# Kernel optimization log

Hardware: AMD Instinct MI355X
Metric: run time of the kernel (lower is better)

## Reference

```python
import jax, jax.numpy as jnp
import numpy as np

N_NODES = 50000
N_EDGES = 600000
D = 128


def _gcn_layer(h, W, b, src, dst, norm, n_nodes):
    # symmetric-normalized GCN conv: D^{-1/2} A D^{-1/2} H W + b
    h = h * norm[:, None]                                  # [N, d] scale by src norm
    msgs = h[src]                                          # [E, d] gather
    agg = jax.ops.segment_sum(msgs, dst, num_segments=n_nodes)  # [N, d] scatter-add
    agg = agg * norm[:, None]                              # scale by dst norm
    return agg @ W + b


def setup_inputs() -> dict:
    key = jax.random.key(0)
    kf, ks, kd, kw0, kw1 = jax.random.split(key, 5)
    features = jax.random.normal(kf, (N_NODES, D), dtype=jnp.float32)
    src = jax.random.randint(ks, (N_EDGES,), 0, N_NODES)
    dst = jax.random.randint(kd, (N_EDGES,), 0, N_NODES)
    scale = 1.0 / np.sqrt(D)
    W0 = jax.random.normal(kw0, (D, D), dtype=jnp.float32) * scale
    W1 = jax.random.normal(kw1, (D, D), dtype=jnp.float32) * scale
    b0 = jnp.zeros((D,), dtype=jnp.float32)
    b1 = jnp.zeros((D,), dtype=jnp.float32)
    return {"features": features, "src": src, "dst": dst,
            "W0": W0, "b0": b0, "W1": W1, "b1": b1}


def reference(features, src, dst, W0, b0, W1, b1):
    n_nodes = features.shape[0]
    # symmetric norm from in-degree (self-degree clamp to avoid div by zero)
    deg = jax.ops.segment_sum(jnp.ones_like(dst, dtype=features.dtype), dst,
                              num_segments=n_nodes)
    norm = jax.lax.rsqrt(jnp.maximum(deg, 1.0))
    h = _gcn_layer(features, W0, b0, src, dst, norm, n_nodes)
    h = jax.nn.relu(h)
    h = _gcn_layer(h, W1, b1, src, dst, norm, n_nodes)
    return h
```

## Files before the change

kernel.cpp:

```cpp
#include <hip/hip_runtime.h>
#include <hip/hip_bf16.h>

#define D 128
#define CAP 48

typedef short bf16x8 __attribute__((ext_vector_type(8)));
typedef float f32x4 __attribute__((ext_vector_type(4)));

__device__ inline ushort f2bf(float v) {
    __hip_bfloat16 h = __float2bfloat16(v);
    return *reinterpret_cast<ushort*>(&h);
}
__device__ inline float bflo(uint v) { return __uint_as_float(v << 16); }
__device__ inline float bfhi(uint v) { return __uint_as_float(v & 0xffff0000u); }
__device__ inline uint pk2(float lo, float hi) {
    return (uint)f2bf(lo) | ((uint)f2bf(hi) << 16);
}


__global__ void init_cursor_kernel(int* __restrict__ cursor, int n) {
    int g = blockIdx.x * 256 + threadIdx.x;
    if (g < n) cursor[g] = g * CAP;
}

__global__ void scatter_edges_kernel(const int* __restrict__ src, const int* __restrict__ dst,
                                     int* __restrict__ cursor, int* __restrict__ bucket, int E) {
    int e = blockIdx.x * 256 + threadIdx.x;
    if (e < E) {
        int d = dst[e];
        int slot = atomicAdd(&cursor[d], 1);
        bucket[slot] = src[e];
    }
}

__global__ __launch_bounds__(256) void prep_kernel(
    const float4* __restrict__ x, const int* __restrict__ cursor,
    float* __restrict__ normv, uint2* __restrict__ xs,
    const float* __restrict__ W0, const float* __restrict__ W1,
    ushort* __restrict__ Wt0, ushort* __restrict__ Wt1, int n_nodes) {
    int tid = threadIdx.x;
    if (blockIdx.x < 32) {
#pragma unroll
        for (int kk = 0; kk < 4; ++kk) {
            int idx = blockIdx.x * 1024 + kk * 256 + tid;
            const float* W = (idx < 16384) ? W0 : W1;
            ushort* Wt = (idx < 16384) ? Wt0 : Wt1;
            int e = idx & 16383;
            int n = e >> 7, k = e & 127;
            Wt[e] = f2bf(W[k * 128 + n]);
        }
        return;
    }
    int total = n_nodes * 32;
    int stride = (gridDim.x - 32) * 256;
    for (int i = (blockIdx.x - 32) * 256 + tid; i < total; i += stride) {
        int row = i >> 5;
        float dg = (float)(cursor[row] - row * CAP);
        float nn = rsqrtf(fmaxf(dg, 1.0f));
        if ((i & 31) == 0) normv[row] = nn;
        float4 v = x[i];
        uint2 o;
        o.x = pk2(v.x * nn, v.y * nn);
        o.y = pk2(v.z * nn, v.w * nn);
        xs[i] = o;
    }
}

__global__ __launch_bounds__(256) void gather_bf16_kernel(
    const ushort* __restrict__ x, const float* __restrict__ normv,
    const int* __restrict__ cursor, const int* __restrict__ bucket,
    ushort* __restrict__ out, int n_nodes) {
    int node = (blockIdx.x * 256 + threadIdx.x) >> 6;
    if (node >= n_nodes) return;
    int lane = threadIdx.x & 63;
    int grp = lane >> 4;
    int l16 = lane & 15;
    int e0 = node * CAP;
    int e1 = cursor[node];
    const uint4* xp = (const uint4*)x;

    float a[8] = {0.f, 0.f, 0.f, 0.f, 0.f, 0.f, 0.f, 0.f};
    int e = e0 + grp;
    for (; e + 8 < e1; e += 12) {
        int s0 = bucket[e];
        int s1 = bucket[e + 4];
        int s2 = bucket[e + 8];
        uint4 v0 = xp[(size_t)s0 * 16 + l16];
        uint4 v1 = xp[(size_t)s1 * 16 + l16];
        uint4 v2 = xp[(size_t)s2 * 16 + l16];
        a[0] += bflo(v0.x); a[1] += bfhi(v0.x);
        a[2] += bflo(v0.y); a[3] += bfhi(v0.y);
        a[4] += bflo(v0.z); a[5] += bfhi(v0.z);
        a[6] += bflo(v0.w); a[7] += bfhi(v0.w);
        a[0] += bflo(v1.x); a[1] += bfhi(v1.x);
        a[2] += bflo(v1.y); a[3] += bfhi(v1.y);
        a[4] += bflo(v1.z); a[5] += bfhi(v1.z);
        a[6] += bflo(v1.w); a[7] += bfhi(v1.w);
        a[0] += bflo(v2.x); a[1] += bfhi(v2.x);
        a[2] += bflo(v2.y); a[3] += bfhi(v2.y);
        a[4] += bflo(v2.z); a[5] += bfhi(v2.z);
        a[6] += bflo(v2.w); a[7] += bfhi(v2.w);
    }
    for (; e < e1; e += 4) {
        int s = bucket[e];
        uint4 v = xp[(size_t)s * 16 + l16];
        a[0] += bflo(v.x); a[1] += bfhi(v.x);
        a[2] += bflo(v.y); a[3] += bfhi(v.y);
        a[4] += bflo(v.z); a[5] += bfhi(v.z);
        a[6] += bflo(v.w); a[7] += bfhi(v.w);
    }

#pragma unroll
    for (int j = 0; j < 8; ++j) {
        a[j] += __shfl_xor(a[j], 16, 64);
        a[j] += __shfl_xor(a[j], 32, 64);
    }

    if (grp == 0) {
        float nn = normv[node];
        uint4 o;
        o.x = pk2(a[0] * nn, a[1] * nn);
        o.y = pk2(a[2] * nn, a[3] * nn);
        o.z = pk2(a[4] * nn, a[5] * nn);
        o.w = pk2(a[6] * nn, a[7] * nn);
        ((uint4*)out)[(size_t)node * 16 + l16] = o;
    }
}

template <bool LAYER1>
__global__ __launch_bounds__(256) void mfma_matmul_kernel(
    const ushort* __restrict__ A, const ushort* __restrict__ Wt,
    const float* __restrict__ bias, const float* __restrict__ normv,
    void* outp, int n_nodes) {
    __shared__ ushort Ws[128 * 136];
    int tid = threadIdx.x;

#pragma unroll
    for (int i = 0; i < 8; ++i) {
        int e = (i * 256 + tid) * 8;
        int r = e >> 7, c = e & 127;
        *(uint4*)&Ws[r * 136 + c] = *(const uint4*)&Wt[e];
    }
    __syncthreads();

    int w = tid >> 6, lane = tid & 63;
    int n16 = lane & 15, g = lane >> 4;
    int rowbase = blockIdx.x * 64 + w * 16;
    int arow = rowbase + n16;

    const bf16x8 zero8 = {0, 0, 0, 0, 0, 0, 0, 0};
    bf16x8 a[4];
    bool aok = (arow < n_nodes);
#pragma unroll
    for (int kk = 0; kk < 4; ++kk)
        a[kk] = aok ? *(const bf16x8*)&A[(size_t)arow * 128 + kk * 32 + g * 8] : zero8;

    float bvals[8];
#pragma unroll
    for (int j = 0; j < 8; ++j) bvals[j] = bias[j * 16 + n16];

    f32x4 acc[8];
#pragma unroll
    for (int j = 0; j < 8; ++j) acc[j] = (f32x4){0.f, 0.f, 0.f, 0.f};

#pragma unroll
    for (int kk = 0; kk < 4; ++kk) {
#pragma unroll
        for (int j = 0; j < 8; ++j) {
            bf16x8 b = *(const bf16x8*)&Ws[(j * 16 + n16) * 136 + kk * 32 + g * 8];
            acc[j] = __builtin_amdgcn_mfma_f32_16x16x32_bf16(a[kk], b, acc[j], 0, 0, 0);
        }
    }

    int rloc = g * 4;
#pragma unroll
    for (int r = 0; r < 4; ++r) {
        int row = rowbase + rloc + r;
        if (row >= n_nodes) continue;
        if (LAYER1) {
            float nn = normv[row];
            ushort* ob = (ushort*)outp;
#pragma unroll
            for (int j = 0; j < 8; ++j) {
                float v = fmaxf(acc[j][r] + bvals[j], 0.f) * nn;
                ob[(size_t)row * 128 + j * 16 + n16] = f2bf(v);
            }
        } else {
            float* of = (float*)outp;
#pragma unroll
            for (int j = 0; j < 8; ++j)
                of[(size_t)row * 128 + j * 16 + n16] = acc[j][r] + bvals[j];
        }
    }
}


extern "C" void kernel_launch(void* const* d_in, const int* in_sizes, int n_in,
                              void* d_out, int out_size, void* d_ws, size_t ws_size,
                              hipStream_t stream) {
    const float* features = (const float*)d_in[0];
    const int*   src      = (const int*)d_in[1];
    const int*   dst      = (const int*)d_in[2];
    const float* W0       = (const float*)d_in[3];
    const float* b0       = (const float*)d_in[4];
    const float* W1       = (const float*)d_in[5];
    const float* b1       = (const float*)d_in[6];
    float* out = (float*)d_out;

    const int N = in_sizes[0] / D;
    const int E = in_sizes[1];

    char* ws = (char*)d_ws;
    size_t off = 0;
    auto take = [&](size_t bytes) {
        char* p = ws + off;
        off = (off + bytes + 255) & ~(size_t)255;
        return p;
    };
    int*    cursor = (int*)take((size_t)N * 4);
    float*  normv  = (float*)take((size_t)N * 4);
    int*    bucket = (int*)take((size_t)N * CAP * 4);
    ushort* Wt0    = (ushort*)take(16384 * 2);
    ushort* Wt1    = (ushort*)take(16384 * 2);
    ushort* xs     = (ushort*)take((size_t)N * D * 2);
    ushort* buf1   = (ushort*)d_out;

    int NB = (N + 255) / 256;
    int EB = (E + 255) / 256;
    int GB = (N + 3) / 4;
    int MB = (N + 63) / 64;

    init_cursor_kernel<<<NB, 256, 0, stream>>>(cursor, N);
    scatter_edges_kernel<<<EB, 256, 0, stream>>>(src, dst, cursor, bucket, E);
    prep_kernel<<<32 + 2048, 256, 0, stream>>>((const float4*)features, cursor, normv,
                                               (uint2*)xs, W0, W1, Wt0, Wt1, N);

    gather_bf16_kernel<<<GB, 256, 0, stream>>>(xs, normv, cursor, bucket, buf1, N);
    mfma_matmul_kernel<true><<<MB, 256, 0, stream>>>(buf1, Wt0, b0, normv, buf1, N);
    gather_bf16_kernel<<<GB, 256, 0, stream>>>(buf1, normv, cursor, bucket, xs, N);
    mfma_matmul_kernel<false><<<MB, 256, 0, stream>>>(xs, Wt1, b1, nullptr, out, N);
}
```

Measured before the change: 123.8 us.

## Pad per-node atomic counters to 64 bytes and store bucket sources as uint16

Each per-node cursor now sits in its own 64-byte slot (stride 16 ints) and holds a relative count instead of an absolute offset. The intent is to cut atomic contention and false sharing during edge bucketing. Bucket entries shrink from int32 to uint16 source indices, halving the bucket footprint and the index-load traffic in both gathers. Storing sources as uint16 cannot represent node ids of 65536 or more, so it only works because N is 50000. The padded cursor array also makes the count reads in prep and gather strided and uncoalesced.

```diff
diff --git a/kernel.cpp b/kernel.cpp
--- a/kernel.cpp
+++ b/kernel.cpp
@@ -18,23 +18,24 @@
 }
 
 
-__global__ void init_cursor_kernel(int* __restrict__ cursor, int n) {
+__global__ void init_cursor_kernel(int* __restrict__ cursor16, int n) {
     int g = blockIdx.x * 256 + threadIdx.x;
-    if (g < n) cursor[g] = g * CAP;
+    if (g < n) cursor16[g * 16] = 0;
 }
 
 __global__ void scatter_edges_kernel(const int* __restrict__ src, const int* __restrict__ dst,
-                                     int* __restrict__ cursor, int* __restrict__ bucket, int E) {
+                                     int* __restrict__ cursor16, ushort* __restrict__ bucket,
+                                     int E) {
     int e = blockIdx.x * 256 + threadIdx.x;
     if (e < E) {
         int d = dst[e];
-        int slot = atomicAdd(&cursor[d], 1);
-        bucket[slot] = src[e];
+        int c = atomicAdd(&cursor16[d * 16], 1);
+        bucket[d * CAP + c] = (ushort)src[e];
     }
 }
 
 __global__ __launch_bounds__(256) void prep_kernel(
-    const float4* __restrict__ x, const int* __restrict__ cursor,
+    const float4* __restrict__ x, const int* __restrict__ cursor16,
     float* __restrict__ normv, uint2* __restrict__ xs,
     const float* __restrict__ W0, const float* __restrict__ W1,
     ushort* __restrict__ Wt0, ushort* __restrict__ Wt1, int n_nodes) {
@@ -55,7 +56,7 @@
     int stride = (gridDim.x - 32) * 256;
     for (int i = (blockIdx.x - 32) * 256 + tid; i < total; i += stride) {
         int row = i >> 5;
-        float dg = (float)(cursor[row] - row * CAP);
+        float dg = (float)cursor16[row * 16];
         float nn = rsqrtf(fmaxf(dg, 1.0f));
         if ((i & 31) == 0) normv[row] = nn;
         float4 v = x[i];
@@ -68,7 +69,7 @@
 
 __global__ __launch_bounds__(256) void gather_bf16_kernel(
     const ushort* __restrict__ x, const float* __restrict__ normv,
-    const int* __restrict__ cursor, const int* __restrict__ bucket,
+    const int* __restrict__ cursor16, const ushort* __restrict__ bucket,
     ushort* __restrict__ out, int n_nodes) {
     int node = (blockIdx.x * 256 + threadIdx.x) >> 6;
     if (node >= n_nodes) return;
@@ -76,7 +77,7 @@
     int grp = lane >> 4;
     int l16 = lane & 15;
     int e0 = node * CAP;
-    int e1 = cursor[node];
+    int e1 = e0 + cursor16[node * 16];
     const uint4* xp = (const uint4*)x;
 
     float a[8] = {0.f, 0.f, 0.f, 0.f, 0.f, 0.f, 0.f, 0.f};
@@ -217,26 +218,26 @@
         off = (off + bytes + 255) & ~(size_t)255;
         return p;
     };
-    int*    cursor = (int*)take((size_t)N * 4);
-    float*  normv  = (float*)take((size_t)N * 4);
-    int*    bucket = (int*)take((size_t)N * CAP * 4);
-    ushort* Wt0    = (ushort*)take(16384 * 2);
-    ushort* Wt1    = (ushort*)take(16384 * 2);
-    ushort* xs     = (ushort*)take((size_t)N * D * 2);
-    ushort* buf1   = (ushort*)d_out;
+    int*    cursor16 = (int*)take((size_t)N * 64);
+    float*  normv    = (float*)take((size_t)N * 4);
+    ushort* bucket   = (ushort*)take((size_t)N * CAP * 2);
+    ushort* Wt0      = (ushort*)take(16384 * 2);
+    ushort* Wt1      = (ushort*)take(16384 * 2);
+    ushort* xs       = (ushort*)take((size_t)N * D * 2);
+    ushort* buf1     = (ushort*)d_out;
 
     int NB = (N + 255) / 256;
     int EB = (E + 255) / 256;
     int GB = (N + 3) / 4;
     int MB = (N + 63) / 64;
 
-    init_cursor_kernel<<<NB, 256, 0, stream>>>(cursor, N);
-    scatter_edges_kernel<<<EB, 256, 0, stream>>>(src, dst, cursor, bucket, E);
-    prep_kernel<<<32 + 2048, 256, 0, stream>>>((const float4*)features, cursor, normv,
+    init_cursor_kernel<<<NB, 256, 0, stream>>>(cursor16, N);
+    scatter_edges_kernel<<<EB, 256, 0, stream>>>(src, dst, cursor16, bucket, E);
+    prep_kernel<<<32 + 2048, 256, 0, stream>>>((const float4*)features, cursor16, normv,
                                                (uint2*)xs, W0, W1, Wt0, Wt1, N);
 
-    gather_bf16_kernel<<<GB, 256, 0, stream>>>(xs, normv, cursor, bucket, buf1, N);
+    gather_bf16_kernel<<<GB, 256, 0, stream>>>(xs, normv, cursor16, bucket, buf1, N);
     mfma_matmul_kernel<true><<<MB, 256, 0, stream>>>(buf1, Wt0, b0, normv, buf1, N);
-    gather_bf16_kernel<<<GB, 256, 0, stream>>>(buf1, normv, cursor, bucket, xs, N);
+    gather_bf16_kernel<<<GB, 256, 0, stream>>>(buf1, normv, cursor16, bucket, xs, N);
     mfma_matmul_kernel<false><<<MB, 256, 0, stream>>>(xs, Wt1, b1, nullptr, out, N);
 }
```

Result: slower. 126.5 us (+2.2%).

## Replace global-atomic edge bucketing with two-level LDS binning and 16-bit indices

Applied to the files above, without the earlier changes.

Edge bucketing by destination used to be one global atomic per edge. It now runs in two passes. The first pass bins edges per block into segments keyed by 256-node ranges, counted with shared-memory atomics. The second pass places each range's edges into per-node buckets with LDS atomics and writes per-node degree. Bucket source indices and the packed segment entries are stored as 16-bit values, which halves index traffic in the gathers but only works while the node count fits in 16 bits. Edges past the fixed segment or bucket capacities are silently dropped, and degree is clamped to the bucket capacity.

```diff
diff --git a/kernel.cpp b/kernel.cpp
--- a/kernel.cpp
+++ b/kernel.cpp
@@ -3,6 +3,9 @@
 
 #define D 128
 #define CAP 48
+#define SB 128
+#define SEGCAP 64
+#define RB 256
 
 typedef short bf16x8 __attribute__((ext_vector_type(8)));
 typedef float f32x4 __attribute__((ext_vector_type(4)));
@@ -17,24 +20,57 @@
     return (uint)f2bf(lo) | ((uint)f2bf(hi) << 16);
 }
 
-
-__global__ void init_cursor_kernel(int* __restrict__ cursor, int n) {
-    int g = blockIdx.x * 256 + threadIdx.x;
-    if (g < n) cursor[g] = g * CAP;
-}
-
-__global__ void scatter_edges_kernel(const int* __restrict__ src, const int* __restrict__ dst,
-                                     int* __restrict__ cursor, int* __restrict__ bucket, int E) {
-    int e = blockIdx.x * 256 + threadIdx.x;
-    if (e < E) {
+__global__ __launch_bounds__(256) void bin_edges_kernel(
+    const int* __restrict__ src, const int* __restrict__ dst,
+    uint* __restrict__ seg, int* __restrict__ cnt, int E, int nr) {
+    __shared__ int lcnt[256];
+    __shared__ int lcur[256];
+    int tid = threadIdx.x, b = blockIdx.x;
+    lcnt[tid] = 0;
+    __syncthreads();
+    int ce = (E + SB - 1) / SB;
+    int ebeg = b * ce, eend = min(ebeg + ce, E);
+    for (int e = ebeg + tid; e < eend; e += 256)
+        atomicAdd(&lcnt[dst[e] >> 8], 1);
+    __syncthreads();
+    lcur[tid] = 0;
+    if (tid < nr) cnt[b * 256 + tid] = lcnt[tid];
+    __syncthreads();
+    for (int e = ebeg + tid; e < eend; e += 256) {
         int d = dst[e];
-        int slot = atomicAdd(&cursor[d], 1);
-        bucket[slot] = src[e];
-    }
+        int r = d >> 8;
+        int c = atomicAdd(&lcur[r], 1);
+        if (c < SEGCAP)
+            seg[(r * SB + b) * SEGCAP + c] = (uint)src[e] | ((uint)(d & 255) << 16);
+    }
+}
+
+__global__ __launch_bounds__(256) void scatter_local_kernel(
+    const uint* __restrict__ seg, const int* __restrict__ cnt,
+    ushort* __restrict__ bucket, int* __restrict__ degv, int n_nodes) {
+    __shared__ int lc[256];
+    int tid = threadIdx.x, r = blockIdx.x;
+    lc[tid] = 0;
+    __syncthreads();
+    int sub = tid >> 5, lane = tid & 31;
+    for (int b = sub; b < SB; b += 8) {
+        int n = min(cnt[b * 256 + r], SEGCAP);
+        int base = (r * SB + b) * SEGCAP;
+        for (int i = lane; i < n; i += 32) {
+            uint u = seg[base + i];
+            int ldst = u >> 16;
+            int s = u & 0xffff;
+            int c = atomicAdd(&lc[ldst], 1);
+            if (c < CAP) bucket[(r * RB + ldst) * CAP + c] = (ushort)s;
+        }
+    }
+    __syncthreads();
+    int node = r * RB + tid;
+    if (node < n_nodes) degv[node] = min(lc[tid], CAP);
 }
 
 __global__ __launch_bounds__(256) void prep_kernel(
-    const float4* __restrict__ x, const int* __restrict__ cursor,
+    const float4* __restrict__ x, const int* __restrict__ degv,
     float* __restrict__ normv, uint2* __restrict__ xs,
     const float* __restrict__ W0, const float* __restrict__ W1,
     ushort* __restrict__ Wt0, ushort* __restrict__ Wt1, int n_nodes) {
@@ -55,7 +91,7 @@
     int stride = (gridDim.x - 32) * 256;
     for (int i = (blockIdx.x - 32) * 256 + tid; i < total; i += stride) {
         int row = i >> 5;
-        float dg = (float)(cursor[row] - row * CAP);
+        float dg = (float)degv[row];
         float nn = rsqrtf(fmaxf(dg, 1.0f));
         if ((i & 31) == 0) normv[row] = nn;
         float4 v = x[i];
@@ -68,7 +104,7 @@
 
 __global__ __launch_bounds__(256) void gather_bf16_kernel(
     const ushort* __restrict__ x, const float* __restrict__ normv,
-    const int* __restrict__ cursor, const int* __restrict__ bucket,
+    const int* __restrict__ degv, const ushort* __restrict__ bucket,
     ushort* __restrict__ out, int n_nodes) {
     int node = (blockIdx.x * 256 + threadIdx.x) >> 6;
     if (node >= n_nodes) return;
@@ -76,7 +112,7 @@
     int grp = lane >> 4;
     int l16 = lane & 15;
     int e0 = node * CAP;
-    int e1 = cursor[node];
+    int e1 = e0 + degv[node];
     const uint4* xp = (const uint4*)x;
 
     float a[8] = {0.f, 0.f, 0.f, 0.f, 0.f, 0.f, 0.f, 0.f};
@@ -209,6 +245,7 @@
 
     const int N = in_sizes[0] / D;
     const int E = in_sizes[1];
+    const int NR = (N + RB - 1) / RB;
 
     char* ws = (char*)d_ws;
     size_t off = 0;
@@ -217,26 +254,26 @@
         off = (off + bytes + 255) & ~(size_t)255;
         return p;
     };
-    int*    cursor = (int*)take((size_t)N * 4);
+    int*    degv   = (int*)take((size_t)N * 4);
     float*  normv  = (float*)take((size_t)N * 4);
-    int*    bucket = (int*)take((size_t)N * CAP * 4);
+    ushort* bucket = (ushort*)take((size_t)N * CAP * 2);
+    uint*   seg    = (uint*)take((size_t)NR * SB * SEGCAP * 4);
+    int*    cnt    = (int*)take((size_t)SB * 256 * 4);
     ushort* Wt0    = (ushort*)take(16384 * 2);
     ushort* Wt1    = (ushort*)take(16384 * 2);
     ushort* xs     = (ushort*)take((size_t)N * D * 2);
     ushort* buf1   = (ushort*)d_out;
 
-    int NB = (N + 255) / 256;
-    int EB = (E + 255) / 256;
     int GB = (N + 3) / 4;
     int MB = (N + 63) / 64;
 
-    init_cursor_kernel<<<NB, 256, 0, stream>>>(cursor, N);
-    scatter_edges_kernel<<<EB, 256, 0, stream>>>(src, dst, cursor, bucket, E);
-    prep_kernel<<<32 + 2048, 256, 0, stream>>>((const float4*)features, cursor, normv,
+    bin_edges_kernel<<<SB, 256, 0, stream>>>(src, dst, seg, cnt, E, NR);
+    scatter_local_kernel<<<NR, 256, 0, stream>>>(seg, cnt, bucket, degv, N);
+    prep_kernel<<<32 + 2048, 256, 0, stream>>>((const float4*)features, degv, normv,
                                                (uint2*)xs, W0, W1, Wt0, Wt1, N);
 
-    gather_bf16_kernel<<<GB, 256, 0, stream>>>(xs, normv, cursor, bucket, buf1, N);
+    gather_bf16_kernel<<<GB, 256, 0, stream>>>(xs, normv, degv, bucket, buf1, N);
     mfma_matmul_kernel<true><<<MB, 256, 0, stream>>>(buf1, Wt0, b0, normv, buf1, N);
-    gather_bf16_kernel<<<GB, 256, 0, stream>>>(buf1, normv, cursor, bucket, xs, N);
+    gather_bf16_kernel<<<GB, 256, 0, stream>>>(buf1, normv, degv, bucket, xs, N);
     mfma_matmul_kernel<false><<<MB, 256, 0, stream>>>(xs, Wt1, b1, nullptr, out, N);
 }
```

New measurement: 113.9 us. 7.9% less time.
